# Performance work log

Measured on AMD Instinct MI355X. Metric: run time of the kernel, lower is better.

## Reference

```python
import jax, jax.numpy as jnp
import numpy as np

N = 100000      # nodes
E = 800000      # directed edges
D_IN = 128      # input features (n_inputs)
HIDDEN = 128    # conf['model']['hidden_size']
D_OUT = 2       # conv2 output classes


def setup_inputs() -> dict:
    key = jax.random.key(0)
    k0, k1, k2, k3 = jax.random.split(key, 4)
    x = jax.random.normal(k0, (N, D_IN), dtype=jnp.float32)
    edge_index = jax.random.randint(k1, (2, E), 0, N, dtype=jnp.int32)
    # Glorot-style init for GCNConv weights, zero bias (PyG defaults)
    s1 = float(np.sqrt(6.0 / (D_IN + HIDDEN)))
    s2 = float(np.sqrt(6.0 / (HIDDEN + D_OUT)))
    W1 = jax.random.uniform(k2, (D_IN, HIDDEN), jnp.float32, -s1, s1)
    b1 = jnp.zeros((HIDDEN,), jnp.float32)
    W2 = jax.random.uniform(k3, (HIDDEN, D_OUT), jnp.float32, -s2, s2)
    b2 = jnp.zeros((D_OUT,), jnp.float32)
    return {"x": x, "edge_index": edge_index, "W1": W1, "b1": b1, "W2": W2, "b2": b2}


def gcn_conv(x, src, dst, W, b):
    """PyG GCNConv: add self-loops, symmetric deg^-1/2 A deg^-1/2 normalization."""
    n = x.shape[0]
    h = x @ W                                                   # [N, F_out]
    ones_e = jnp.ones((src.shape[0],), h.dtype)
    # degree with self-loops (init to 1)
    deg = jnp.ones((n,), h.dtype).at[dst].add(ones_e)           # [N]
    dinv = 1.0 / jnp.sqrt(deg)
    norm = (dinv[src] * dinv[dst])[:, None]                     # [E, 1]
    # self-loop contribution: norm_ii = dinv_i^2; then scatter edge messages
    out = (h * (dinv * dinv)[:, None]).at[dst].add(h[src] * norm)
    return out + b


def reference(x, edge_index, W1, b1, W2, b2):
    src, dst = edge_index[0], edge_index[1]
    h = jax.nn.relu(gcn_conv(x, src, dst, W1, b1))
    return gcn_conv(h, src, dst, W2, b2)                        # [N, 2]
```

## Files before the change

### kernel.cpp

```cpp
#include <hip/hip_runtime.h>
#include <hip/hip_bf16.h>


#define D1 128
#define BSH 8
#define BSZ (1 << BSH)
#define NBMAX 1024
#define CHA 2048

typedef __attribute__((ext_vector_type(8))) short short8;
typedef __attribute__((ext_vector_type(4))) float floatx4;

__device__ __forceinline__ unsigned short f2bf(float f) {
    unsigned u = __float_as_uint(f);
    u += 0x7fff + ((u >> 16) & 1);
    return (unsigned short)(u >> 16);
}
__device__ __forceinline__ float bflo(unsigned u) { return __uint_as_float(u << 16); }
__device__ __forceinline__ float bfhi(unsigned u) { return __uint_as_float(u & 0xffff0000u); }
__device__ __forceinline__ int clampN(int s, int N) {
    return (int)min((unsigned)s, (unsigned)N);
}

__global__ void k_init(const float* __restrict__ W1, unsigned short* __restrict__ W1t,
                       int* __restrict__ bcur, unsigned short* __restrict__ h1s,
                       float* __restrict__ h2s, int N) {
    int i = blockIdx.x * 256 + threadIdx.x;
    if (i < NBMAX) bcur[i] = 0;
    if (i < D1) h1s[(size_t)N * D1 + i] = 0;
    if (i < 2)  h2s[(size_t)N * 2 + i] = 0.f;
    if (i < D1 * D1) {
        int c = i >> 7, k = i & 127;
        W1t[c * D1 + k] = f2bf(W1[k * D1 + c]);
    }
}

__global__ __launch_bounds__(256) void k_binA(
    const int* __restrict__ src, const int* __restrict__ dst,
    int* __restrict__ bcur, unsigned* __restrict__ packed, int E, int nbuck, int CAP)
{
    __shared__ int hist[NBMAX];
    __shared__ int cur[NBMAX];
    const int t = threadIdx.x;
    const int e0 = blockIdx.x * CHA;
    const int e1 = min(e0 + CHA, E);

    for (int i = t; i < nbuck; i += 256) hist[i] = 0;
    __syncthreads();
    for (int i = e0 + t; i < e1; i += 256)
        atomicAdd(&hist[dst[i] >> BSH], 1);
    __syncthreads();
    for (int i = t; i < nbuck; i += 256)
        cur[i] = (hist[i] > 0) ? atomicAdd(&bcur[i], hist[i]) : 0;
    __syncthreads();
    for (int i = e0 + t; i < e1; i += 256) {
        int d = dst[i];
        int b = d >> BSH;
        int pos = atomicAdd(&cur[b], 1);
        if (pos < CAP)
            packed[(size_t)b * CAP + pos] = ((unsigned)src[i] << BSH) | (unsigned)(d & (BSZ - 1));
    }
}

__global__ __launch_bounds__(BSZ) void k_binB(
    const int* __restrict__ bcur, const unsigned* __restrict__ packed,
    int2* __restrict__ rp, float* __restrict__ dinv,
    int* __restrict__ esrc, int* __restrict__ order, int N, int CAP)
{
    __shared__ int lh[BSZ];
    __shared__ int lcur[BSZ];
    __shared__ int wsum[BSZ / 64];
    __shared__ int dbin[64];
    __shared__ int dcur[64];

    const int t = threadIdx.x;
    const int s = blockIdx.x << BSH;
    const int n = min(BSZ, N - s);
    const int base = blockIdx.x * CAP;
    const int cnt = min(bcur[blockIdx.x], CAP);

    lh[t] = 0;
    if (t < 64) dbin[t] = 0;
    __syncthreads();
    for (int i = t; i < cnt; i += BSZ)
        atomicAdd(&lh[packed[base + i] & (BSZ - 1)], 1);
    __syncthreads();

    const int deg = lh[t];
    const int pdeg = (deg + 3) & ~3;

    int inc = pdeg;
#pragma unroll
    for (int off = 1; off < 64; off <<= 1) {
        int u = __shfl_up(inc, off);
        if ((t & 63) >= off) inc += u;
    }
    if ((t & 63) == 63) wsum[t >> 6] = inc;
    __syncthreads();
    if (t < BSZ / 64) {
        int w = wsum[t];
#pragma unroll
        for (int off = 1; off < BSZ / 64; off <<= 1) {
            int u = __shfl_up(w, off, BSZ / 64);
            if ((t & (BSZ / 64 - 1)) >= off) w += u;
        }
        wsum[t] = w;
    }
    __syncthreads();
    int excl = ((t >> 6) ? wsum[(t >> 6) - 1] : 0) + inc - pdeg;

    if (t < n) {
        rp[s + t] = make_int2(base + excl, deg);
        dinv[s + t] = rsqrtf(1.0f + (float)deg);
        atomicAdd(&dbin[63 - min(deg, 63)], 1);
        for (int k = deg; k < pdeg; ++k) {
            int p = excl + k;
            if (p < CAP) esrc[base + p] = N;
        }
    }
    lcur[t] = excl;
    __syncthreads();

    for (int i = t; i < cnt; i += BSZ) {
        unsigned p = packed[base + i];
        int ld = (int)(p & (BSZ - 1));
        int pos = atomicAdd(&lcur[ld], 1);
        if (pos < CAP) esrc[base + pos] = (int)(p >> BSH);
    }

    __syncthreads();
    if (t < 64) {
        int dv = dbin[t];
        int dinc = dv;
#pragma unroll
        for (int off = 1; off < 64; off <<= 1) {
            int u = __shfl_up(dinc, off);
            if (t >= off) dinc += u;
        }
        dcur[t] = dinc - dv;
    }
    __syncthreads();
    if (t < n) {
        int b = 63 - min(deg, 63);
        int pos = atomicAdd(&dcur[b], 1);
        order[s + pos] = s + t;
    }
}

#define BMM 128
__global__ __launch_bounds__(512) void k_gemm1(
    const float* __restrict__ x, const unsigned short* __restrict__ W1t,
    const float* __restrict__ dinv, unsigned short* __restrict__ h1s, int N)
{
    __shared__ unsigned short Xs[BMM][136];
    __shared__ unsigned short Ws[D1][136];

    const int t = threadIdx.x;
    const int row0 = blockIdx.x * BMM;

#pragma unroll
    for (int i = 0; i < 4; ++i) {
        int idx = t + 512 * i;
        int r = idx >> 4, c8 = idx & 15;
        short8 v = ((const short8*)W1t)[r * 16 + c8];
        *(short8*)&Ws[r][c8 * 8] = v;
    }
#pragma unroll
    for (int i = 0; i < 4; ++i) {
        int idx = t + 512 * i;
        int r = idx >> 4, c8 = idx & 15;
        int row = row0 + r;
        short8 v8 = (short8)0;
        if (row < N) {
            const float* p = x + (size_t)row * D1 + c8 * 8;
            float4 f0 = *(const float4*)p;
            float4 f1 = *(const float4*)(p + 4);
            v8[0] = (short)f2bf(f0.x); v8[1] = (short)f2bf(f0.y);
            v8[2] = (short)f2bf(f0.z); v8[3] = (short)f2bf(f0.w);
            v8[4] = (short)f2bf(f1.x); v8[5] = (short)f2bf(f1.y);
            v8[6] = (short)f2bf(f1.z); v8[7] = (short)f2bf(f1.w);
        }
        *(short8*)&Xs[r][c8 * 8] = v8;
    }
    __syncthreads();

    const int w = t >> 6;
    const int l = t & 63;
    const int m = l & 15;
    const int q = l >> 4;

    floatx4 acc[8];
#pragma unroll
    for (int c = 0; c < 8; ++c) acc[c] = (floatx4)0.0f;

#pragma unroll
    for (int ks = 0; ks < 4; ++ks) {
        short8 a = *(const short8*)&Xs[16 * w + m][ks * 32 + q * 8];
#pragma unroll
        for (int c = 0; c < 8; ++c) {
            short8 b = *(const short8*)&Ws[c * 16 + m][ks * 32 + q * 8];
            acc[c] = __builtin_amdgcn_mfma_f32_16x16x32_bf16(a, b, acc[c], 0, 0, 0);
        }
    }

    __syncthreads();

#pragma unroll
    for (int r = 0; r < 4; ++r) {
        int rt = 16 * w + q * 4 + r;
        int row = row0 + rt;
        float di = (row < N) ? dinv[row] : 0.f;
#pragma unroll
        for (int c = 0; c < 8; ++c)
            Xs[rt][c * 16 + m] = f2bf(acc[c][r] * di);
    }
    __syncthreads();

#pragma unroll
    for (int i = 0; i < 4; ++i) {
        int idx = t + 512 * i;
        int r = idx >> 4, c8 = idx & 15;
        int row = row0 + r;
        if (row < N)
            *(short8*)&h1s[(size_t)row * D1 + c8 * 8] = *(const short8*)&Xs[r][c8 * 8];
    }
}

#define ACC8(A, v) \
    A[0] += bflo(v.x); A[1] += bfhi(v.x); \
    A[2] += bflo(v.y); A[3] += bfhi(v.y); \
    A[4] += bflo(v.z); A[5] += bfhi(v.z); \
    A[6] += bflo(v.w); A[7] += bfhi(v.w);

__global__ __launch_bounds__(256) void k_agg1_gemm2(
    const int2* __restrict__ rp, const int* __restrict__ esrc,
    const int* __restrict__ order,
    const float* __restrict__ dinv, const unsigned short* __restrict__ h1s,
    const float* __restrict__ b1, const float* __restrict__ W2,
    float* __restrict__ h2s, int N)
{
    int gid = blockIdx.x * 256 + threadIdx.x;
    int grp = gid >> 4;
    if (grp >= N) return;
    int node = order[grp];
    int lane = gid & 15;

    const uint4* h1v = (const uint4*)h1s;
    const int4*  ev  = (const int4*)esrc;

    uint4 u = h1v[(size_t)node * 16 + lane];
    float accA[8], accB[8];
    accA[0] = bflo(u.x); accA[1] = bfhi(u.x);
    accA[2] = bflo(u.y); accA[3] = bfhi(u.y);
    accA[4] = bflo(u.z); accA[5] = bfhi(u.z);
    accA[6] = bflo(u.w); accA[7] = bfhi(u.w);
#pragma unroll
    for (int j = 0; j < 8; ++j) accB[j] = 0.f;

    int2 r = rp[node];
    int beg = r.x;
    int end4 = beg + ((r.y + 3) & ~3);

    for (int e = beg; e < end4; e += 8) {
        int q = e >> 2;
        int4 i0 = ev[q];
        int4 i1 = ev[q + 1];
        bool c1 = (e + 4) < end4;
        int s0 = clampN(i0.x, N), s1 = clampN(i0.y, N);
        int s2 = clampN(i0.z, N), s3 = clampN(i0.w, N);
        int s4 = c1 ? clampN(i1.x, N) : N, s5 = c1 ? clampN(i1.y, N) : N;
        int s6 = c1 ? clampN(i1.z, N) : N, s7 = c1 ? clampN(i1.w, N) : N;
        uint4 v0 = h1v[(size_t)s0 * 16 + lane];
        uint4 v1 = h1v[(size_t)s1 * 16 + lane];
        uint4 v2 = h1v[(size_t)s2 * 16 + lane];
        uint4 v3 = h1v[(size_t)s3 * 16 + lane];
        uint4 v4 = h1v[(size_t)s4 * 16 + lane];
        uint4 v5 = h1v[(size_t)s5 * 16 + lane];
        uint4 v6 = h1v[(size_t)s6 * 16 + lane];
        uint4 v7 = h1v[(size_t)s7 * 16 + lane];
        ACC8(accA, v0) ACC8(accB, v1) ACC8(accA, v2) ACC8(accB, v3)
        ACC8(accA, v4) ACC8(accB, v5) ACC8(accA, v6) ACC8(accB, v7)
    }

    float di = dinv[node];
    const float4* b1v = (const float4*)b1;
    float4 bbA = b1v[lane * 2 + 0];
    float4 bbB = b1v[lane * 2 + 1];
    float a[8];
    a[0] = fmaxf((accA[0] + accB[0]) * di + bbA.x, 0.f);
    a[1] = fmaxf((accA[1] + accB[1]) * di + bbA.y, 0.f);
    a[2] = fmaxf((accA[2] + accB[2]) * di + bbA.z, 0.f);
    a[3] = fmaxf((accA[3] + accB[3]) * di + bbA.w, 0.f);
    a[4] = fmaxf((accA[4] + accB[4]) * di + bbB.x, 0.f);
    a[5] = fmaxf((accA[5] + accB[5]) * di + bbB.y, 0.f);
    a[6] = fmaxf((accA[6] + accB[6]) * di + bbB.z, 0.f);
    a[7] = fmaxf((accA[7] + accB[7]) * di + bbB.w, 0.f);

    const float4* W2v = (const float4*)W2;
    float p0 = 0.f, p1 = 0.f;
#pragma unroll
    for (int j2 = 0; j2 < 4; ++j2) {
        float4 wv = W2v[lane * 4 + j2];
        p0 += a[j2 * 2] * wv.x + a[j2 * 2 + 1] * wv.z;
        p1 += a[j2 * 2] * wv.y + a[j2 * 2 + 1] * wv.w;
    }

#pragma unroll
    for (int off = 8; off > 0; off >>= 1) {
        p0 += __shfl_xor(p0, off);
        p1 += __shfl_xor(p1, off);
    }
    if (lane == 0) {
        h2s[(size_t)node * 2 + 0] = p0 * di;
        h2s[(size_t)node * 2 + 1] = p1 * di;
    }
}

__global__ void k_gather2(const int2* __restrict__ rp, const int* __restrict__ esrc,
                          const float* __restrict__ h2s, const float* __restrict__ dinv,
                          const float* __restrict__ b2, float* __restrict__ out, int N)
{
    int i = blockIdx.x * 256 + threadIdx.x;
    if (i >= N) return;
    const float2* h2v = (const float2*)h2s;
    const int4* ev = (const int4*)esrc;
    float2 h = h2v[i];
    float o0a = h.x, o1a = h.y;
    float o0b = 0.f, o1b = 0.f;
    int2 r = rp[i];
    int beg = r.x;
    int end4 = beg + ((r.y + 3) & ~3);
    for (int e = beg; e < end4; e += 16) {
        int q = e >> 2;
        int4 i0 = ev[q];
        int4 i1 = ev[q + 1];
        int4 i2 = ev[q + 2];
        int4 i3 = ev[q + 3];
        bool c1 = (e + 4) < end4, c2 = (e + 8) < end4, c3 = (e + 12) < end4;
        int s0 = clampN(i0.x, N), s1 = clampN(i0.y, N);
        int s2 = clampN(i0.z, N), s3 = clampN(i0.w, N);
        int s4 = c1 ? clampN(i1.x, N) : N, s5 = c1 ? clampN(i1.y, N) : N;
        int s6 = c1 ? clampN(i1.z, N) : N, s7 = c1 ? clampN(i1.w, N) : N;
        int s8 = c2 ? clampN(i2.x, N) : N, s9 = c2 ? clampN(i2.y, N) : N;
        int sa = c2 ? clampN(i2.z, N) : N, sb = c2 ? clampN(i2.w, N) : N;
        int sc = c3 ? clampN(i3.x, N) : N, sd = c3 ? clampN(i3.y, N) : N;
        int se = c3 ? clampN(i3.z, N) : N, sf = c3 ? clampN(i3.w, N) : N;
        float2 v0 = h2v[s0], v1 = h2v[s1], v2 = h2v[s2], v3 = h2v[s3];
        float2 v4 = h2v[s4], v5 = h2v[s5], v6 = h2v[s6], v7 = h2v[s7];
        float2 v8 = h2v[s8], v9 = h2v[s9], va = h2v[sa], vb = h2v[sb];
        float2 vc = h2v[sc], vd = h2v[sd], ve = h2v[se], vf = h2v[sf];
        o0a += v0.x + v2.x + v4.x + v6.x + v8.x + va.x + vc.x + ve.x;
        o1a += v0.y + v2.y + v4.y + v6.y + v8.y + va.y + vc.y + ve.y;
        o0b += v1.x + v3.x + v5.x + v7.x + v9.x + vb.x + vd.x + vf.x;
        o1b += v1.y + v3.y + v5.y + v7.y + v9.y + vb.y + vd.y + vf.y;
    }
    float di = dinv[i];
    ((float2*)out)[i] = make_float2((o0a + o0b) * di + b2[0], (o1a + o1b) * di + b2[1]);
}

extern "C" void kernel_launch(void* const* d_in, const int* in_sizes, int n_in,
                              void* d_out, int out_size, void* d_ws, size_t ws_size,
                              hipStream_t stream)
{
    const float* x  = (const float*)d_in[0];
    const int*   ei = (const int*)d_in[1];
    const float* W1 = (const float*)d_in[2];
    const float* b1 = (const float*)d_in[3];
    const float* W2 = (const float*)d_in[4];
    const float* b2 = (const float*)d_in[5];
    float* out = (float*)d_out;

    const int N = in_sizes[0] / D1;
    const int E = in_sizes[1] / 2;
    const int* src = ei;
    const int* dst = ei + E;

    const int nbuck = (N + BSZ - 1) >> BSH;
    const int avg = (E + nbuck - 1) / nbuck;
    const int CAP = (2 * avg + 3 * BSZ + 63) & ~63;

    char* w = (char*)d_ws;
    auto alloc = [&](size_t bytes) -> char* {
        char* r = w;
        w += (bytes + 63) & ~(size_t)63;
        return r;
    };
    unsigned short* h1s = (unsigned short*)alloc((size_t)(N + 1) * D1 * 2);
    unsigned short* W1t = (unsigned short*)alloc((size_t)D1 * D1 * 2);
    float* h2s    = (float*)alloc((size_t)(N + 1) * 2 * 4);
    float* dinv   = (float*)alloc((size_t)N * 4);
    int2*  rp     = (int2*)alloc((size_t)N * 8);
    int*   order  = (int*)alloc((size_t)N * 4);
    int*   bcur   = (int*)alloc(NBMAX * 4);
    unsigned* packed = (unsigned*)alloc((size_t)nbuck * CAP * 4);
    int*   esrc   = (int*)alloc(((size_t)nbuck * CAP + 256) * 4);

    k_init <<<(D1 * D1 + 255) / 256, 256, 0, stream>>>(W1, W1t, bcur, h1s, h2s, N);
    k_binA <<<(E + CHA - 1) / CHA, 256, 0, stream>>>(src, dst, bcur, packed, E, nbuck, CAP);
    k_binB <<<nbuck, BSZ, 0, stream>>>(bcur, packed, rp, dinv, esrc, order, N, CAP);

    k_gemm1<<<(N + BMM - 1) / BMM, 512, 0, stream>>>(x, W1t, dinv, h1s, N);

    k_agg1_gemm2<<<(N * 16 + 255) / 256, 256, 0, stream>>>(rp, esrc, order, dinv, h1s, b1, W2, h2s, N);

    k_gather2<<<(N + 255) / 256, 256, 0, stream>>>(rp, esrc, h2s, dinv, b2, out, N);
}
```

Before: 180.8 us.

## Fuse GEMM1 with edge binning in one launch, move dinv scaling into aggregation

GEMM1 no longer scales rows by the source dinv, so it no longer depends on the degree computation. This lets it run as interleaved blocks in the same launch as the first edge-binning pass, so the compute-bound GEMM overlaps the atomic-heavy binning and one kernel launch is removed. In exchange, the aggregation kernel now loads dinv for every gathered neighbor and does an extra multiply per element. dinv gets a padded zero entry so dummy edges are handled correctly.

```diff
diff --git a/kernel.cpp b/kernel.cpp
--- a/kernel.cpp
+++ b/kernel.cpp
@@ -7,6 +7,7 @@
 #define BSZ (1 << BSH)
 #define NBMAX 1024
 #define CHA 2048
+#define BMM 128
 
 typedef __attribute__((ext_vector_type(8))) short short8;
 typedef __attribute__((ext_vector_type(4))) float floatx4;
@@ -24,139 +25,66 @@
 
 __global__ void k_init(const float* __restrict__ W1, unsigned short* __restrict__ W1t,
                        int* __restrict__ bcur, unsigned short* __restrict__ h1s,
-                       float* __restrict__ h2s, int N) {
+                       float* __restrict__ h2s, float* __restrict__ dinv, int N) {
     int i = blockIdx.x * 256 + threadIdx.x;
     if (i < NBMAX) bcur[i] = 0;
     if (i < D1) h1s[(size_t)N * D1 + i] = 0;
     if (i < 2)  h2s[(size_t)N * 2 + i] = 0.f;
+    if (i == 0) dinv[N] = 0.f;
     if (i < D1 * D1) {
         int c = i >> 7, k = i & 127;
         W1t[c * D1 + k] = f2bf(W1[k * D1 + c]);
     }
 }
 
-__global__ __launch_bounds__(256) void k_binA(
+__global__ __launch_bounds__(512) void k_gemm1_binA(
+    const float* __restrict__ x, const unsigned short* __restrict__ W1t,
+    unsigned short* __restrict__ h1s,
     const int* __restrict__ src, const int* __restrict__ dst,
-    int* __restrict__ bcur, unsigned* __restrict__ packed, int E, int nbuck, int CAP)
+    int* __restrict__ bcur, unsigned* __restrict__ packed,
+    int N, int E, int nbuck, int CAP, int GA, int GG)
 {
-    __shared__ int hist[NBMAX];
-    __shared__ int cur[NBMAX];
+    __shared__ __align__(16) char smem[2 * BMM * 136 * 2];
+
+    const int b = blockIdx.x;
+    const int m2 = 2 * min(GA, GG);
+    bool isA;
+    int bid;
+    if (b < m2)            { isA = (b & 1); bid = b >> 1; }
+    else if (GA <= GG)     { isA = false;   bid = min(GA, GG) + (b - m2); }
+    else                   { isA = true;    bid = min(GA, GG) + (b - m2); }
+
+    if (isA) {
+        int* hist = (int*)smem;
+        int* cur  = hist + NBMAX;
+        const int t = threadIdx.x;
+        const int e0 = bid * CHA;
+        const int e1 = min(e0 + CHA, E);
+
+        for (int i = t; i < nbuck; i += 512) hist[i] = 0;
+        __syncthreads();
+        for (int i = e0 + t; i < e1; i += 512)
+            atomicAdd(&hist[dst[i] >> BSH], 1);
+        __syncthreads();
+        for (int i = t; i < nbuck; i += 512)
+            cur[i] = (hist[i] > 0) ? atomicAdd(&bcur[i], hist[i]) : 0;
+        __syncthreads();
+        for (int i = e0 + t; i < e1; i += 512) {
+            int d = dst[i];
+            int bk = d >> BSH;
+            int pos = atomicAdd(&cur[bk], 1);
+            if (pos < CAP)
+                packed[(size_t)bk * CAP + pos] =
+                    ((unsigned)src[i] << BSH) | (unsigned)(d & (BSZ - 1));
+        }
+        return;
+    }
+
+    unsigned short (*Xs)[136] = (unsigned short(*)[136])smem;
+    unsigned short (*Ws)[136] = (unsigned short(*)[136])(smem + BMM * 136 * 2);
+
     const int t = threadIdx.x;
-    const int e0 = blockIdx.x * CHA;
-    const int e1 = min(e0 + CHA, E);
-
-    for (int i = t; i < nbuck; i += 256) hist[i] = 0;
-    __syncthreads();
-    for (int i = e0 + t; i < e1; i += 256)
-        atomicAdd(&hist[dst[i] >> BSH], 1);
-    __syncthreads();
-    for (int i = t; i < nbuck; i += 256)
-        cur[i] = (hist[i] > 0) ? atomicAdd(&bcur[i], hist[i]) : 0;
-    __syncthreads();
-    for (int i = e0 + t; i < e1; i += 256) {
-        int d = dst[i];
-        int b = d >> BSH;
-        int pos = atomicAdd(&cur[b], 1);
-        if (pos < CAP)
-            packed[(size_t)b * CAP + pos] = ((unsigned)src[i] << BSH) | (unsigned)(d & (BSZ - 1));
-    }
-}
-
-__global__ __launch_bounds__(BSZ) void k_binB(
-    const int* __restrict__ bcur, const unsigned* __restrict__ packed,
-    int2* __restrict__ rp, float* __restrict__ dinv,
-    int* __restrict__ esrc, int* __restrict__ order, int N, int CAP)
-{
-    __shared__ int lh[BSZ];
-    __shared__ int lcur[BSZ];
-    __shared__ int wsum[BSZ / 64];
-    __shared__ int dbin[64];
-    __shared__ int dcur[64];
-
-    const int t = threadIdx.x;
-    const int s = blockIdx.x << BSH;
-    const int n = min(BSZ, N - s);
-    const int base = blockIdx.x * CAP;
-    const int cnt = min(bcur[blockIdx.x], CAP);
-
-    lh[t] = 0;
-    if (t < 64) dbin[t] = 0;
-    __syncthreads();
-    for (int i = t; i < cnt; i += BSZ)
-        atomicAdd(&lh[packed[base + i] & (BSZ - 1)], 1);
-    __syncthreads();
-
-    const int deg = lh[t];
-    const int pdeg = (deg + 3) & ~3;
-
-    int inc = pdeg;
-#pragma unroll
-    for (int off = 1; off < 64; off <<= 1) {
-        int u = __shfl_up(inc, off);
-        if ((t & 63) >= off) inc += u;
-    }
-    if ((t & 63) == 63) wsum[t >> 6] = inc;
-    __syncthreads();
-    if (t < BSZ / 64) {
-        int w = wsum[t];
-#pragma unroll
-        for (int off = 1; off < BSZ / 64; off <<= 1) {
-            int u = __shfl_up(w, off, BSZ / 64);
-            if ((t & (BSZ / 64 - 1)) >= off) w += u;
-        }
-        wsum[t] = w;
-    }
-    __syncthreads();
-    int excl = ((t >> 6) ? wsum[(t >> 6) - 1] : 0) + inc - pdeg;
-
-    if (t < n) {
-        rp[s + t] = make_int2(base + excl, deg);
-        dinv[s + t] = rsqrtf(1.0f + (float)deg);
-        atomicAdd(&dbin[63 - min(deg, 63)], 1);
-        for (int k = deg; k < pdeg; ++k) {
-            int p = excl + k;
-            if (p < CAP) esrc[base + p] = N;
-        }
-    }
-    lcur[t] = excl;
-    __syncthreads();
-
-    for (int i = t; i < cnt; i += BSZ) {
-        unsigned p = packed[base + i];
-        int ld = (int)(p & (BSZ - 1));
-        int pos = atomicAdd(&lcur[ld], 1);
-        if (pos < CAP) esrc[base + pos] = (int)(p >> BSH);
-    }
-
-    __syncthreads();
-    if (t < 64) {
-        int dv = dbin[t];
-        int dinc = dv;
-#pragma unroll
-        for (int off = 1; off < 64; off <<= 1) {
-            int u = __shfl_up(dinc, off);
-            if (t >= off) dinc += u;
-        }
-        dcur[t] = dinc - dv;
-    }
-    __syncthreads();
-    if (t < n) {
-        int b = 63 - min(deg, 63);
-        int pos = atomicAdd(&dcur[b], 1);
-        order[s + pos] = s + t;
-    }
-}
-
-#define BMM 128
-__global__ __launch_bounds__(512) void k_gemm1(
-    const float* __restrict__ x, const unsigned short* __restrict__ W1t,
-    const float* __restrict__ dinv, unsigned short* __restrict__ h1s, int N)
-{
-    __shared__ unsigned short Xs[BMM][136];
-    __shared__ unsigned short Ws[D1][136];
-
-    const int t = threadIdx.x;
-    const int row0 = blockIdx.x * BMM;
+    const int row0 = bid * BMM;
 
 #pragma unroll
     for (int i = 0; i < 4; ++i) {
@@ -198,8 +126,8 @@
         short8 a = *(const short8*)&Xs[16 * w + m][ks * 32 + q * 8];
 #pragma unroll
         for (int c = 0; c < 8; ++c) {
-            short8 b = *(const short8*)&Ws[c * 16 + m][ks * 32 + q * 8];
-            acc[c] = __builtin_amdgcn_mfma_f32_16x16x32_bf16(a, b, acc[c], 0, 0, 0);
+            short8 bb = *(const short8*)&Ws[c * 16 + m][ks * 32 + q * 8];
+            acc[c] = __builtin_amdgcn_mfma_f32_16x16x32_bf16(a, bb, acc[c], 0, 0, 0);
         }
     }
 
@@ -208,11 +136,9 @@
 #pragma unroll
     for (int r = 0; r < 4; ++r) {
         int rt = 16 * w + q * 4 + r;
-        int row = row0 + rt;
-        float di = (row < N) ? dinv[row] : 0.f;
 #pragma unroll
         for (int c = 0; c < 8; ++c)
-            Xs[rt][c * 16 + m] = f2bf(acc[c][r] * di);
+            Xs[rt][c * 16 + m] = f2bf(acc[c][r]);
     }
     __syncthreads();
 
@@ -226,11 +152,96 @@
     }
 }
 
-#define ACC8(A, v) \
-    A[0] += bflo(v.x); A[1] += bfhi(v.x); \
-    A[2] += bflo(v.y); A[3] += bfhi(v.y); \
-    A[4] += bflo(v.z); A[5] += bfhi(v.z); \
-    A[6] += bflo(v.w); A[7] += bfhi(v.w);
+__global__ __launch_bounds__(BSZ) void k_binB(
+    const int* __restrict__ bcur, const unsigned* __restrict__ packed,
+    int2* __restrict__ rp, float* __restrict__ dinv,
+    int* __restrict__ esrc, int* __restrict__ order, int N, int CAP)
+{
+    __shared__ int lh[BSZ];
+    __shared__ int lcur[BSZ];
+    __shared__ int wsum[BSZ / 64];
+    __shared__ int dbin[64];
+    __shared__ int dcur[64];
+
+    const int t = threadIdx.x;
+    const int s = blockIdx.x << BSH;
+    const int n = min(BSZ, N - s);
+    const int base = blockIdx.x * CAP;
+    const int cnt = min(bcur[blockIdx.x], CAP);
+
+    lh[t] = 0;
+    if (t < 64) dbin[t] = 0;
+    __syncthreads();
+    for (int i = t; i < cnt; i += BSZ)
+        atomicAdd(&lh[packed[base + i] & (BSZ - 1)], 1);
+    __syncthreads();
+
+    const int deg = lh[t];
+    const int pdeg = (deg + 3) & ~3;
+
+    int inc = pdeg;
+#pragma unroll
+    for (int off = 1; off < 64; off <<= 1) {
+        int u = __shfl_up(inc, off);
+        if ((t & 63) >= off) inc += u;
+    }
+    if ((t & 63) == 63) wsum[t >> 6] = inc;
+    __syncthreads();
+    if (t < BSZ / 64) {
+        int w = wsum[t];
+#pragma unroll
+        for (int off = 1; off < BSZ / 64; off <<= 1) {
+            int u = __shfl_up(w, off, BSZ / 64);
+            if ((t & (BSZ / 64 - 1)) >= off) w += u;
+        }
+        wsum[t] = w;
+    }
+    __syncthreads();
+    int excl = ((t >> 6) ? wsum[(t >> 6) - 1] : 0) + inc - pdeg;
+
+    if (t < n) {
+        rp[s + t] = make_int2(base + excl, deg);
+        dinv[s + t] = rsqrtf(1.0f + (float)deg);
+        atomicAdd(&dbin[63 - min(deg, 63)], 1);
+        for (int k = deg; k < pdeg; ++k) {
+            int p = excl + k;
+            if (p < CAP) esrc[base + p] = N;
+        }
+    }
+    lcur[t] = excl;
+    __syncthreads();
+
+    for (int i = t; i < cnt; i += BSZ) {
+        unsigned p = packed[base + i];
+        int ld = (int)(p & (BSZ - 1));
+        int pos = atomicAdd(&lcur[ld], 1);
+        if (pos < CAP) esrc[base + pos] = (int)(p >> BSH);
+    }
+
+    __syncthreads();
+    if (t < 64) {
+        int dv = dbin[t];
+        int dinc = dv;
+#pragma unroll
+        for (int off = 1; off < 64; off <<= 1) {
+            int u = __shfl_up(dinc, off);
+            if (t >= off) dinc += u;
+        }
+        dcur[t] = dinc - dv;
+    }
+    __syncthreads();
+    if (t < n) {
+        int b = 63 - min(deg, 63);
+        int pos = atomicAdd(&dcur[b], 1);
+        order[s + pos] = s + t;
+    }
+}
+
+#define ACC8F(A, v, d) \
+    A[0] += bflo(v.x) * d; A[1] += bfhi(v.x) * d; \
+    A[2] += bflo(v.y) * d; A[3] += bfhi(v.y) * d; \
+    A[4] += bflo(v.z) * d; A[5] += bfhi(v.z) * d; \
+    A[6] += bflo(v.w) * d; A[7] += bfhi(v.w) * d;
 
 __global__ __launch_bounds__(256) void k_agg1_gemm2(
     const int2* __restrict__ rp, const int* __restrict__ esrc,
@@ -248,12 +259,13 @@
     const uint4* h1v = (const uint4*)h1s;
     const int4*  ev  = (const int4*)esrc;
 
+    float di = dinv[node];
     uint4 u = h1v[(size_t)node * 16 + lane];
     float accA[8], accB[8];
-    accA[0] = bflo(u.x); accA[1] = bfhi(u.x);
-    accA[2] = bflo(u.y); accA[3] = bfhi(u.y);
-    accA[4] = bflo(u.z); accA[5] = bfhi(u.z);
-    accA[6] = bflo(u.w); accA[7] = bfhi(u.w);
+    accA[0] = bflo(u.x) * di; accA[1] = bfhi(u.x) * di;
+    accA[2] = bflo(u.y) * di; accA[3] = bfhi(u.y) * di;
+    accA[4] = bflo(u.z) * di; accA[5] = bfhi(u.z) * di;
+    accA[6] = bflo(u.w) * di; accA[7] = bfhi(u.w) * di;
 #pragma unroll
     for (int j = 0; j < 8; ++j) accB[j] = 0.f;
 
@@ -270,6 +282,8 @@
         int s2 = clampN(i0.z, N), s3 = clampN(i0.w, N);
         int s4 = c1 ? clampN(i1.x, N) : N, s5 = c1 ? clampN(i1.y, N) : N;
         int s6 = c1 ? clampN(i1.z, N) : N, s7 = c1 ? clampN(i1.w, N) : N;
+        float d0 = dinv[s0], d1 = dinv[s1], d2 = dinv[s2], d3 = dinv[s3];
+        float d4 = dinv[s4], d5 = dinv[s5], d6 = dinv[s6], d7 = dinv[s7];
         uint4 v0 = h1v[(size_t)s0 * 16 + lane];
         uint4 v1 = h1v[(size_t)s1 * 16 + lane];
         uint4 v2 = h1v[(size_t)s2 * 16 + lane];
@@ -278,11 +292,10 @@
         uint4 v5 = h1v[(size_t)s5 * 16 + lane];
         uint4 v6 = h1v[(size_t)s6 * 16 + lane];
         uint4 v7 = h1v[(size_t)s7 * 16 + lane];
-        ACC8(accA, v0) ACC8(accB, v1) ACC8(accA, v2) ACC8(accB, v3)
-        ACC8(accA, v4) ACC8(accB, v5) ACC8(accA, v6) ACC8(accB, v7)
-    }
-
-    float di = dinv[node];
+        ACC8F(accA, v0, d0) ACC8F(accB, v1, d1) ACC8F(accA, v2, d2) ACC8F(accB, v3, d3)
+        ACC8F(accA, v4, d4) ACC8F(accB, v5, d5) ACC8F(accA, v6, d6) ACC8F(accB, v7, d7)
+    }
+
     const float4* b1v = (const float4*)b1;
     float4 bbA = b1v[lane * 2 + 0];
     float4 bbB = b1v[lane * 2 + 1];
@@ -388,19 +401,21 @@
     unsigned short* h1s = (unsigned short*)alloc((size_t)(N + 1) * D1 * 2);
     unsigned short* W1t = (unsigned short*)alloc((size_t)D1 * D1 * 2);
     float* h2s    = (float*)alloc((size_t)(N + 1) * 2 * 4);
-    float* dinv   = (float*)alloc((size_t)N * 4);
+    float* dinv   = (float*)alloc((size_t)(N + 1) * 4);
     int2*  rp     = (int2*)alloc((size_t)N * 8);
     int*   order  = (int*)alloc((size_t)N * 4);
     int*   bcur   = (int*)alloc(NBMAX * 4);
     unsigned* packed = (unsigned*)alloc((size_t)nbuck * CAP * 4);
     int*   esrc   = (int*)alloc(((size_t)nbuck * CAP + 256) * 4);
 
-    k_init <<<(D1 * D1 + 255) / 256, 256, 0, stream>>>(W1, W1t, bcur, h1s, h2s, N);
-    k_binA <<<(E + CHA - 1) / CHA, 256, 0, stream>>>(src, dst, bcur, packed, E, nbuck, CAP);
+    const int GA = (E + CHA - 1) / CHA;
+    const int GG = (N + BMM - 1) / BMM;
+
+    k_init <<<(D1 * D1 + 255) / 256, 256, 0, stream>>>(W1, W1t, bcur, h1s, h2s, dinv, N);
+    k_gemm1_binA<<<GA + GG, 512, 0, stream>>>(x, W1t, h1s, src, dst, bcur, packed,
+                                              N, E, nbuck, CAP, GA, GG);
     k_binB <<<nbuck, BSZ, 0, stream>>>(bcur, packed, rp, dinv, esrc, order, N, CAP);
 
-    k_gemm1<<<(N + BMM - 1) / BMM, 512, 0, stream>>>(x, W1t, dinv, h1s, N);
-
     k_agg1_gemm2<<<(N * 16 + 255) / 256, 256, 0, stream>>>(rp, esrc, order, dinv, h1s, b1, W2, h2s, N);
 
     k_gather2<<<(N + 255) / 256, 256, 0, stream>>>(rp, esrc, h2s, dinv, b2, out, N);
```

Result: no change. 179.8 us, median of 2 (-0.6%).
